# Kernel optimization log

Measured on AMD Instinct MI355X. Metric: run time of the kernel, lower is better.

Reference implementation:

```python
import jax, jax.numpy as jnp
import numpy as np
import math

NUM_BUCKETS = 32
MAX_DISTANCE = 128


def _relative_position_bucket(relative_position):
    # Unidirectional (bidirectional=False): rp = max(-relative_position, 0)
    rp = jnp.maximum(-relative_position, 0)
    max_exact = NUM_BUCKETS // 2  # 16
    is_small = rp < max_exact
    rp_f = jnp.maximum(rp, 1).astype(jnp.float32)
    large = max_exact + (
        jnp.log(rp_f / max_exact) / math.log(MAX_DISTANCE / max_exact)
        * (NUM_BUCKETS - max_exact)
    ).astype(jnp.int32)
    large = jnp.minimum(large, NUM_BUCKETS - 1)
    return jnp.where(is_small, rp, large)


def _t5_rel_bias(bias_table, T):
    # bias_table: [num_buckets, n_heads] -> [1, n_heads, T, T]
    ctx = jnp.arange(T, dtype=jnp.int32)[:, None]
    mem = jnp.arange(T, dtype=jnp.int32)[None, :]
    buckets = _relative_position_bucket(mem - ctx)  # [T, T]
    values = bias_table[buckets]  # [T, T, H]
    return jnp.transpose(values, (2, 0, 1))[None]  # [1, H, T, T]


def setup_inputs() -> dict:
    key = jax.random.key(0)
    ks = jax.random.split(key, 6)
    B, T, C, H = 2, 2048, 1024, 16
    x = jax.random.normal(ks[0], (B, T, C), dtype=jnp.float32)
    W_attn = jax.random.normal(ks[1], (C, 3 * C), dtype=jnp.float32) * 0.02
    b_attn = jnp.zeros((3 * C,), dtype=jnp.float32)
    W_proj = jax.random.normal(ks[2], (C, C), dtype=jnp.float32) * 0.02
    b_proj = jnp.zeros((C,), dtype=jnp.float32)
    bias_table = jax.random.normal(ks[3], (NUM_BUCKETS, H), dtype=jnp.float32) * 0.02
    return {"x": x, "W_attn": W_attn, "b_attn": b_attn,
            "W_proj": W_proj, "b_proj": b_proj, "bias_table": bias_table}


def reference(x, W_attn, b_attn, W_proj, b_proj, bias_table):
    B, T, C = x.shape
    H = bias_table.shape[1]
    D = C // H
    qkv = x @ W_attn + b_attn  # [B, T, 3C]
    q, k, v = jnp.split(qkv, 3, axis=-1)
    # [B, T, C] -> [B, H, T, D]
    q = q.reshape(B, T, H, D).transpose(0, 2, 1, 3)
    k = k.reshape(B, T, H, D).transpose(0, 2, 1, 3)
    v = v.reshape(B, T, H, D).transpose(0, 2, 1, 3)
    rel_bias = _t5_rel_bias(bias_table, T)  # [1, H, T, T]
    att = jnp.einsum('bhtd,bhsd->bhts', q, k) * (1.0 / math.sqrt(D))
    att = att + rel_bias
    causal = jnp.tril(jnp.ones((T, T), dtype=bool))
    att = jnp.where(causal, att, -jnp.inf)
    att = jax.nn.softmax(att, axis=-1)
    y = jnp.einsum('bhts,bhsd->bhtd', att, v)  # [B, H, T, D]
    y = y.transpose(0, 2, 1, 3).reshape(B, T, C)
    return y @ W_proj + b_proj
```

## Files before the change

kernel.cpp:

```cpp
#include <hip/hip_runtime.h>
#include <hip/hip_bf16.h>
#include <math.h>

typedef __attribute__((ext_vector_type(4))) float f32x4;
typedef __attribute__((ext_vector_type(16))) float f32x16;
typedef __attribute__((ext_vector_type(8))) __bf16 bf16x8;
typedef __attribute__((ext_vector_type(4))) __bf16 bf16x4;
typedef __attribute__((ext_vector_type(4))) unsigned int u32x4;
typedef __attribute__((ext_vector_type(2))) unsigned int u32x2;

#define DEVI __device__ __forceinline__

DEVI f32x4 mfma16(bf16x8 a, bf16x8 b, f32x4 c) {
  return __builtin_amdgcn_mfma_f32_16x16x32_bf16(a, b, c, 0, 0, 0);
}
DEVI f32x16 mfma32(bf16x8 a, bf16x8 b, f32x16 c) {
  return __builtin_amdgcn_mfma_f32_32x32x16_bf16(a, b, c, 0, 0, 0);
}

DEVI void gload16(const void* g, void* l) {
  __builtin_amdgcn_global_load_lds(
      (const __attribute__((address_space(1))) void*)g,
      (__attribute__((address_space(3))) void*)l, 16, 0, 0);
}

DEVI float exp2a(float x) {
  float r;
  asm("v_exp_f32 %0, %1" : "=v"(r) : "v"(x));
  return r;
}
DEVI unsigned cvtpk(float lo, float hi) {
  unsigned r;
  asm("v_cvt_pk_bf16_f32 %0, %1, %2" : "=v"(r) : "v"(lo), "v"(hi));
  return r;
}

#define LOG2E 1.4426950408889634f
#define QSCALE 0.18033688011110793f
#define FIXMAX 8.0f

__global__ __launch_bounds__(256) void prep_k(
    const float* __restrict__ x, const float* __restrict__ W_attn,
    const float* __restrict__ W_proj, const float* __restrict__ bt,
    __bf16* __restrict__ xb, __bf16* __restrict__ WaT,
    __bf16* __restrict__ WpT, float* __restrict__ tbl) {
  __shared__ float tile[32][33];
  int bid = blockIdx.x;
  const int t = threadIdx.x;
  if (bid < 4096) {
    int i = (bid * 256 + t) * 4;
    float4 v = *(const float4*)&x[i];
    bf16x4 o = {(__bf16)v.x, (__bf16)v.y, (__bf16)v.z, (__bf16)v.w};
    *(bf16x4*)&xb[i] = o;
    return;
  }
  bid -= 4096;
  if (bid < 4096) {
    const float* in;
    __bf16* out;
    int Cc, bx, by;
    if (bid < 3072) {
      in = W_attn; out = WaT; Cc = 3072; bx = bid % 96; by = bid / 96;
    } else {
      int b2 = bid - 3072;
      in = W_proj; out = WpT; Cc = 1024; bx = b2 % 32; by = b2 / 32;
    }
    const int R = 1024;
    int tx = t & 31, ty = t >> 5;
    int xcol = bx * 32 + tx;
    for (int r = ty; r < 32; r += 8)
      tile[r][tx] = in[(size_t)(by * 32 + r) * Cc + xcol];
    __syncthreads();
    int xo = by * 32 + tx;
    for (int r = ty; r < 32; r += 8)
      out[(size_t)(bx * 32 + r) * R + xo] = (__bf16)tile[tx][r];
    return;
  }
  bid -= 4096;
  int idx = bid * 256 + t;
  int h = idx >> 11, rp = idx & 2047;
  int bucket;
  if (rp < 16) {
    bucket = rp;
  } else {
    float v = (logf((float)rp * 0.0625f) / 2.0794415416798357f) * 16.0f;
    bucket = 16 + (int)v;
    if (bucket > 31) bucket = 31;
  }
  tbl[idx] = bt[bucket * 16 + h] * LOG2E;
}

__global__ __launch_bounds__(512, 2) void gemm_qkv(
    const __bf16* __restrict__ A, const __bf16* __restrict__ BT,
    const float* __restrict__ bias,
    __bf16* __restrict__ qb, __bf16* __restrict__ kb, __bf16* __restrict__ vtb) {
  __shared__ __align__(16) char lAm[65536];
  __shared__ __align__(16) char lBm[65536];
  const int t = threadIdx.x, w = t >> 6, lane = t & 63;
  const int wm = w >> 2, wn = w & 3;
  const int m0 = blockIdx.x * 256, n0 = blockIdx.y * 256;
  const int rA = lane & 15;
  const int aoff = rA * 128 + (((lane >> 4) * 16) ^ ((rA & 4) ? 32 : 0));
  const int bro = (wn & 1) * 8192;

  int srw[2], scl[2];
#pragma unroll
  for (int r = 0; r < 2; ++r) {
    int d = r * 8192 + w * 1024 + lane * 16;
    int lg = d ^ ((lane & 32) ? 32 : 0);
    srw[r] = lg >> 7;
    scl[r] = (lg & 127) >> 1;
  }

  f32x4 acc[8][4] = {};

  auto STG = [&](int buf, const __bf16* src, int rows0, int kk0, char* opm,
                 int half) {
#pragma unroll
    for (int r = 0; r < 2; ++r)
      gload16(src + (size_t)(rows0 + half * 128 + srw[r]) * 1024 + kk0 + scl[r],
              opm + buf * 32768 + half * 16384 + r * 8192 + w * 1024);
  };
  auto STGALL = [&](int buf, int kk0) {
    STG(buf, A, m0, kk0, lAm, 0);
    STG(buf, A, m0, kk0, lAm, 1);
    STG(buf, BT, n0, kk0, lBm, 0);
    STG(buf, BT, n0, kk0, lBm, 1);
  };

  STGALL(0, 0);
  asm volatile("s_waitcnt vmcnt(0)" ::: "memory");
  __builtin_amdgcn_s_barrier();

  for (int kt = 0; kt < 16; ++kt) {
    const int c = kt & 1;
    const char* Ah = lAm + c * 32768 + wm * 16384;
    const char* Bh = lBm + c * 32768 + (wn >> 1) * 16384 + bro;
    bf16x8 af[4][2], bfr[2][2];

#pragma unroll
    for (int i = 0; i < 4; ++i) {
      af[i][0] = *(const bf16x8*)(Ah + i * 2048 + aoff);
      af[i][1] = *(const bf16x8*)(Ah + i * 2048 + 64 + aoff);
    }
#pragma unroll
    for (int j = 0; j < 2; ++j) {
      bfr[j][0] = *(const bf16x8*)(Bh + j * 2048 + aoff);
      bfr[j][1] = *(const bf16x8*)(Bh + j * 2048 + 64 + aoff);
    }
    if (kt + 1 < 16) STGALL(c ^ 1, (kt + 1) * 64);
    __builtin_amdgcn_s_barrier();
    __builtin_amdgcn_s_setprio(1);
#pragma unroll
    for (int i = 0; i < 4; ++i)
#pragma unroll
      for (int j = 0; j < 2; ++j)
#pragma unroll
        for (int kc = 0; kc < 2; ++kc)
          acc[i][j] = mfma16(af[i][kc], bfr[j][kc], acc[i][j]);
    __builtin_amdgcn_s_setprio(0);
    __builtin_amdgcn_s_barrier();

#pragma unroll
    for (int j = 0; j < 2; ++j) {
      bfr[j][0] = *(const bf16x8*)(Bh + (2 + j) * 2048 + aoff);
      bfr[j][1] = *(const bf16x8*)(Bh + (2 + j) * 2048 + 64 + aoff);
    }
    __builtin_amdgcn_s_barrier();
    __builtin_amdgcn_s_setprio(1);
#pragma unroll
    for (int i = 0; i < 4; ++i)
#pragma unroll
      for (int j = 0; j < 2; ++j)
#pragma unroll
        for (int kc = 0; kc < 2; ++kc)
          acc[i][2 + j] = mfma16(af[i][kc], bfr[j][kc], acc[i][2 + j]);
    __builtin_amdgcn_s_setprio(0);
    __builtin_amdgcn_s_barrier();

#pragma unroll
    for (int i = 0; i < 4; ++i) {
      af[i][0] = *(const bf16x8*)(Ah + (4 + i) * 2048 + aoff);
      af[i][1] = *(const bf16x8*)(Ah + (4 + i) * 2048 + 64 + aoff);
    }
    __builtin_amdgcn_s_barrier();
    __builtin_amdgcn_s_setprio(1);
#pragma unroll
    for (int i = 0; i < 4; ++i)
#pragma unroll
      for (int j = 0; j < 2; ++j)
#pragma unroll
        for (int kc = 0; kc < 2; ++kc)
          acc[4 + i][2 + j] = mfma16(af[i][kc], bfr[j][kc], acc[4 + i][2 + j]);
    __builtin_amdgcn_s_setprio(0);
    __builtin_amdgcn_s_barrier();

#pragma unroll
    for (int j = 0; j < 2; ++j) {
      bfr[j][0] = *(const bf16x8*)(Bh + j * 2048 + aoff);
      bfr[j][1] = *(const bf16x8*)(Bh + j * 2048 + 64 + aoff);
    }
    __builtin_amdgcn_s_barrier();
    __builtin_amdgcn_s_setprio(1);
#pragma unroll
    for (int i = 0; i < 4; ++i)
#pragma unroll
      for (int j = 0; j < 2; ++j)
#pragma unroll
        for (int kc = 0; kc < 2; ++kc)
          acc[4 + i][j] = mfma16(af[i][kc], bfr[j][kc], acc[4 + i][j]);
    __builtin_amdgcn_s_setprio(0);
    if (kt + 1 < 16) asm volatile("s_waitcnt vmcnt(0)" ::: "memory");
    __builtin_amdgcn_s_barrier();
  }

#pragma unroll
  for (int j = 0; j < 4; ++j) {
    int n = n0 + wn * 64 + j * 16 + rA;
    float bv = bias[n];
    int sec = n >> 10, nn = n & 1023;
    int h = nn >> 6, d = nn & 63;
#pragma unroll
    for (int i = 0; i < 8; ++i) {
#pragma unroll
      for (int e = 0; e < 4; ++e) {
        int m = m0 + wm * 128 + i * 16 + (lane >> 4) * 4 + e;
        float v = acc[i][j][e] + bv;
        int b = m >> 11, tt = m & 2047;
        if (sec == 0)
          qb[(((size_t)(b * 16 + h)) * 2048 + tt) * 64 + d] = (__bf16)(v * QSCALE);
        else if (sec == 1)
          kb[(((size_t)(b * 16 + h)) * 2048 + tt) * 64 + d] = (__bf16)v;
        else
          vtb[(((size_t)(b * 16 + h)) * 64 + d) * 2048 + tt] = (__bf16)v;
      }
    }
  }
}

__global__ __launch_bounds__(256) void gemm_proj(
    const __bf16* __restrict__ A, const __bf16* __restrict__ BT,
    const float* __restrict__ bias, float* __restrict__ outF,
    int M, int N, int K) {
  __shared__ __align__(16) __bf16 lA[2][64 * 32];
  __shared__ __align__(16) __bf16 lB[2][128 * 32];
  const int t = threadIdx.x;
  const int w = t >> 6, lane = t & 63;
  const int m0 = blockIdx.x * 64, n0 = blockIdx.y * 128;
  const int wr = (w >> 1) * 32, wc = (w & 1) * 64;

  f32x4 acc[2][4] = {};

  const int rA = lane & 15;
  const int kk = (lane >> 4) * 8;

  auto STAGE = [&](int buf, int k0) {
    {
      int row = t >> 2, cc = t & 3;
      gload16(A + (size_t)(m0 + row) * K + k0 + cc * 8,
              &lA[buf][(w * 64) * 8]);
    }
#pragma unroll
    for (int r = 0; r < 2; ++r) {
      int c = r * 256 + t;
      int row = c >> 2, cc = c & 3;
      gload16(BT + (size_t)(n0 + row) * K + k0 + cc * 8,
              &lB[buf][(r * 256 + w * 64) * 8]);
    }
  };

  STAGE(0, 0);
  int cur = 0;
  for (int k0 = 0; k0 < K; k0 += 32, cur ^= 1) {
    __syncthreads();
    if (k0 + 32 < K) STAGE(cur ^ 1, k0 + 32);
    bf16x8 af[2], bfr[4];
#pragma unroll
    for (int i = 0; i < 2; ++i)
      af[i] = *(const bf16x8*)&lA[cur][(wr + i * 16 + rA) * 32 + kk];
#pragma unroll
    for (int j = 0; j < 4; ++j)
      bfr[j] = *(const bf16x8*)&lB[cur][(wc + j * 16 + rA) * 32 + kk];
#pragma unroll
    for (int i = 0; i < 2; ++i)
#pragma unroll
      for (int j = 0; j < 4; ++j)
        acc[i][j] = mfma16(af[i], bfr[j], acc[i][j]);
  }

  const int colb = n0 + wc + rA;
  const int rowb = m0 + wr + (lane >> 4) * 4;
#pragma unroll
  for (int j = 0; j < 4; ++j) {
    int n = colb + j * 16;
    float bv = bias[n];
#pragma unroll
    for (int i = 0; i < 2; ++i) {
#pragma unroll
      for (int e = 0; e < 4; ++e) {
        int m = rowb + i * 16 + e;
        outF[(size_t)m * N + n] = acc[i][j][e] + bv;
      }
    }
  }
}

__global__ __launch_bounds__(256) void attn_k(
    const __bf16* __restrict__ q, const __bf16* __restrict__ k,
    const __bf16* __restrict__ vt, const float* __restrict__ tbl,
    __bf16* __restrict__ y) {
  __shared__ __align__(16) char smem[2 * 8192 + 2 * 8192 + 2 * 768];
  float* lbuf = (float*)(smem + 32768);

  const int t = threadIdx.x, w = t >> 6, lane = t & 63;
  const int bh = blockIdx.x, b = bh >> 4, h = bh & 15;
  const int qt64 = 31 - blockIdx.y;
  const int qs = w >> 1, ks = w & 1;
  const int ncol = lane & 31, hi = lane >> 5;
  const int swl = ncol & 7;

  const __bf16* qp = q + (size_t)bh * 2048 * 64;
  const __bf16* kp = k + (size_t)bh * 2048 * 64;
  const __bf16* vp = vt + (size_t)bh * 64 * 2048;
  const float* tb = tbl + h * 2048;
  const float bconst = tb[2047] - FIXMAX;

  bf16x8 qf[4];
  {
    const __bf16* qr = qp + (size_t)(qt64 * 64 + qs * 32 + ncol) * 64 + hi * 8;
#pragma unroll
    for (int dc = 0; dc < 4; ++dc) qf[dc] = *(const bf16x8*)(qr + dc * 16);
  }

  f32x16 O0 = {}, O1 = {};
  float lsum = 0.f;
  const int ibase = 95 + 32 * (qs - ks) - 4 * hi + ncol;

  auto STAGE = [&](int buf, int jt) {
#pragma unroll
    for (int r = 0; r < 2; ++r) {
      int c = r * 256 + t;
      int row = c >> 3, cc = c & 7;
      int sc = cc ^ (row & 7);
      gload16(kp + (size_t)(jt * 64 + row) * 64 + sc * 8,
              smem + buf * 8192 + (r * 256 + w * 64) * 16);
      gload16(vp + (size_t)row * 2048 + jt * 64 + sc * 8,
              smem + 16384 + buf * 8192 + (r * 256 + w * 64) * 16);
    }
    int dtj = qt64 - jt;
    if (dtj < 3 && t < 192) {
      int rb = dtj * 64 - 95 + t;
      lbuf[buf * 192 + t] = tb[rb < 0 ? 0 : rb] - FIXMAX;
    }
  };

  STAGE(0, 0);
  int cur = 0;
  for (int jt = 0; jt <= qt64; ++jt, cur ^= 1) {
    const int dt = qt64 - jt;
    const int rel = 2 * dt + qs - ks;
    __syncthreads();
    if (jt < qt64) STAGE(cur ^ 1, jt + 1);
    if (rel < 0) continue;

    const char* Kc = smem + cur * 8192;
    const char* Vc = smem + 16384 + cur * 8192;
    const float* lbc = lbuf + cur * 192;

    f32x16 s;
    if (rel >= 5) {
#pragma unroll
      for (int r = 0; r < 16; ++r) s[r] = bconst;
    } else {
#pragma unroll
      for (int r = 0; r < 16; ++r) {
        int cr8 = (r & 3) + 8 * (r >> 2);
        float v = lbc[ibase - cr8];
        if (rel == 0 && ncol < cr8 + 4 * hi) v = -1e30f;
        s[r] = v;
      }
    }
    const char* Kb = Kc + (ks * 32 + ncol) * 128;
#pragma unroll
    for (int dc = 0; dc < 4; ++dc) {
      bf16x8 kf = *(const bf16x8*)(Kb + (((dc * 2 + hi) ^ swl) << 4));
      s = mfma32(kf, qf[dc], s);
    }
    float p[16];
#pragma unroll
    for (int r = 0; r < 16; ++r) {
      p[r] = exp2a(s[r]);
      lsum += p[r];
    }
#pragma unroll
    for (int s16 = 0; s16 < 2; ++s16) {
      unsigned we0 = cvtpk(p[8 * s16 + 0], p[8 * s16 + 1]);
      unsigned we1 = cvtpk(p[8 * s16 + 2], p[8 * s16 + 3]);
      unsigned wo0 = cvtpk(p[8 * s16 + 4], p[8 * s16 + 5]);
      unsigned wo1 = cvtpk(p[8 * s16 + 6], p[8 * s16 + 7]);
      u32x2 r0 = __builtin_amdgcn_permlane32_swap(we0, wo0, false, false);
      u32x2 r1 = __builtin_amdgcn_permlane32_swap(we1, wo1, false, false);
      u32x4 aw = {r0[0], r1[0], r0[1], r1[1]};
      bf16x8 af = __builtin_bit_cast(bf16x8, aw);
#pragma unroll
      for (int db = 0; db < 2; ++db) {
        const char* Vb = Vc + (db * 32 + ncol) * 128;
        bf16x8 vf = *(const bf16x8*)(Vb +
            ((((ks * 2 + s16) * 2 + hi) ^ swl) << 4));
        if (db == 0) O0 = mfma32(af, vf, O0);
        else         O1 = mfma32(af, vf, O1);
      }
    }
  }

  lsum += __shfl_xor(lsum, 32);
  __syncthreads();
  float* ls = (float*)(smem + 32768);
  if (ks) {
    char* dst = smem + qs * 8192 + lane * 128;
#pragma unroll
    for (int c = 0; c < 4; ++c) {
      f32x4 v0 = {O0[4 * c], O0[4 * c + 1], O0[4 * c + 2], O0[4 * c + 3]};
      *(f32x4*)(dst + ((c ^ swl) << 4)) = v0;
      f32x4 v1 = {O1[4 * c], O1[4 * c + 1], O1[4 * c + 2], O1[4 * c + 3]};
      *(f32x4*)(dst + (((c + 4) ^ swl) << 4)) = v1;
    }
    ls[qs * 64 + lane] = lsum;
  }
  __syncthreads();
  if (!ks) {
    lsum += ls[qs * 64 + lane];
    const char* src = smem + qs * 8192 + lane * 128;
#pragma unroll
    for (int c = 0; c < 4; ++c) {
      f32x4 v0 = *(const f32x4*)(src + ((c ^ swl) << 4));
      f32x4 v1 = *(const f32x4*)(src + (((c + 4) ^ swl) << 4));
#pragma unroll
      for (int e = 0; e < 4; ++e) {
        O0[4 * c + e] += v0[e];
        O1[4 * c + e] += v1[e];
      }
    }
    float rinv = 1.0f / lsum;
#pragma unroll
    for (int r = 0; r < 16; ++r) {
      int cr = (r & 3) + 8 * (r >> 2) + 4 * hi;
      float ri = __shfl(rinv, cr);
      int row = qt64 * 64 + qs * 32 + cr;
      size_t base = ((size_t)(b * 2048 + row)) * 1024 + h * 64 + ncol;
      y[base]      = (__bf16)(O0[r] * ri);
      y[base + 32] = (__bf16)(O1[r] * ri);
    }
  }
}


extern "C" void kernel_launch(void* const* d_in, const int* in_sizes, int n_in,
                              void* d_out, int out_size, void* d_ws, size_t ws_size,
                              hipStream_t stream) {
  const float* x = (const float*)d_in[0];
  const float* W_attn = (const float*)d_in[1];
  const float* b_attn = (const float*)d_in[2];
  const float* W_proj = (const float*)d_in[3];
  const float* b_proj = (const float*)d_in[4];
  const float* bias_table = (const float*)d_in[5];
  float* out = (float*)d_out;

  char* ws = (char*)d_ws;
  __bf16* xb   = (__bf16*)(ws + 0);
  __bf16* WaT  = (__bf16*)(ws + 8388608);
  __bf16* WpT  = (__bf16*)(ws + 14680064);
  __bf16* qb   = (__bf16*)(ws + 16777216);
  __bf16* kb   = (__bf16*)(ws + 25165824);
  __bf16* vtb  = (__bf16*)(ws + 33554432);
  __bf16* yb   = (__bf16*)(ws + 41943040);
  float*  tbl  = (float*)(ws + 50331648);

  prep_k<<<8320, 256, 0, stream>>>(x, W_attn, W_proj, bias_table,
                                   xb, WaT, WpT, tbl);
  gemm_qkv<<<dim3(16, 12), 512, 0, stream>>>(xb, WaT, b_attn, qb, kb, vtb);
  attn_k<<<dim3(32, 32), 256, 0, stream>>>(qb, kb, vtb, tbl, yb);
  gemm_proj<<<dim3(64, 8), 256, 0, stream>>>(yb, WpT, b_proj, out,
                                             4096, 1024, 1024);
}
```

Measured before the change: 133.3 us.

## Use full XOR-8 LDS swizzle and keep B fragments in registers for QKV GEMM

Changes the LDS swizzle of the QKV GEMM from a 2-way XOR to an XOR over all 8 16-byte chunks keyed by row, applied both in the global-to-LDS staging addresses and in the fragment reads, to cut LDS bank conflicts. It keeps B fragments for columns 0-1 in registers (b01) instead of reloading them, which removes one LDS reload and one barrier per k-step. The launch bound drops the 2-blocks-per-SM hint so the compiler may use more registers, at the cost of possible lower occupancy.

```diff
diff --git a/kernel.cpp b/kernel.cpp
--- a/kernel.cpp
+++ b/kernel.cpp
@@ -90,7 +90,7 @@
   tbl[idx] = bt[bucket * 16 + h] * LOG2E;
 }
 
-__global__ __launch_bounds__(512, 2) void gemm_qkv(
+__global__ __launch_bounds__(512) void gemm_qkv(
     const __bf16* __restrict__ A, const __bf16* __restrict__ BT,
     const float* __restrict__ bias,
     __bf16* __restrict__ qb, __bf16* __restrict__ kb, __bf16* __restrict__ vtb) {
@@ -100,16 +100,16 @@
   const int wm = w >> 2, wn = w & 3;
   const int m0 = blockIdx.x * 256, n0 = blockIdx.y * 256;
   const int rA = lane & 15;
-  const int aoff = rA * 128 + (((lane >> 4) * 16) ^ ((rA & 4) ? 32 : 0));
+  const int sw7 = rA & 7;
+  const int ckbase = lane >> 4;
   const int bro = (wn & 1) * 8192;
 
   int srw[2], scl[2];
 #pragma unroll
   for (int r = 0; r < 2; ++r) {
     int d = r * 8192 + w * 1024 + lane * 16;
-    int lg = d ^ ((lane & 32) ? 32 : 0);
-    srw[r] = lg >> 7;
-    scl[r] = (lg & 127) >> 1;
+    srw[r] = d >> 7;
+    scl[r] = (((d >> 4) & 7) ^ (srw[r] & 7)) * 8;
   }
 
   f32x4 acc[8][4] = {};
@@ -127,6 +127,9 @@
     STG(buf, BT, n0, kk0, lBm, 0);
     STG(buf, BT, n0, kk0, lBm, 1);
   };
+  auto FOFF = [&](int rl, int kc) {
+    return rl * 128 + (((ckbase + kc * 4) ^ sw7) << 4);
+  };
 
   STGALL(0, 0);
   asm volatile("s_waitcnt vmcnt(0)" ::: "memory");
@@ -136,18 +139,18 @@
     const int c = kt & 1;
     const char* Ah = lAm + c * 32768 + wm * 16384;
     const char* Bh = lBm + c * 32768 + (wn >> 1) * 16384 + bro;
-    bf16x8 af[4][2], bfr[2][2];
-
-#pragma unroll
-    for (int i = 0; i < 4; ++i) {
-      af[i][0] = *(const bf16x8*)(Ah + i * 2048 + aoff);
-      af[i][1] = *(const bf16x8*)(Ah + i * 2048 + 64 + aoff);
-    }
-#pragma unroll
-    for (int j = 0; j < 2; ++j) {
-      bfr[j][0] = *(const bf16x8*)(Bh + j * 2048 + aoff);
-      bfr[j][1] = *(const bf16x8*)(Bh + j * 2048 + 64 + aoff);
-    }
+    bf16x8 af[4][2], b01[2][2], b23[2][2];
+
+#pragma unroll
+    for (int i = 0; i < 4; ++i)
+#pragma unroll
+      for (int kc = 0; kc < 2; ++kc)
+        af[i][kc] = *(const bf16x8*)(Ah + FOFF(i * 16 + rA, kc));
+#pragma unroll
+    for (int j = 0; j < 2; ++j)
+#pragma unroll
+      for (int kc = 0; kc < 2; ++kc)
+        b01[j][kc] = *(const bf16x8*)(Bh + FOFF(j * 16 + rA, kc));
     if (kt + 1 < 16) STGALL(c ^ 1, (kt + 1) * 64);
     __builtin_amdgcn_s_barrier();
     __builtin_amdgcn_s_setprio(1);
@@ -157,15 +160,15 @@
       for (int j = 0; j < 2; ++j)
 #pragma unroll
         for (int kc = 0; kc < 2; ++kc)
-          acc[i][j] = mfma16(af[i][kc], bfr[j][kc], acc[i][j]);
+          acc[i][j] = mfma16(af[i][kc], b01[j][kc], acc[i][j]);
     __builtin_amdgcn_s_setprio(0);
     __builtin_amdgcn_s_barrier();
 
 #pragma unroll
-    for (int j = 0; j < 2; ++j) {
-      bfr[j][0] = *(const bf16x8*)(Bh + (2 + j) * 2048 + aoff);
-      bfr[j][1] = *(const bf16x8*)(Bh + (2 + j) * 2048 + 64 + aoff);
-    }
+    for (int j = 0; j < 2; ++j)
+#pragma unroll
+      for (int kc = 0; kc < 2; ++kc)
+        b23[j][kc] = *(const bf16x8*)(Bh + FOFF((2 + j) * 16 + rA, kc));
     __builtin_amdgcn_s_barrier();
     __builtin_amdgcn_s_setprio(1);
 #pragma unroll
@@ -174,15 +177,15 @@
       for (int j = 0; j < 2; ++j)
 #pragma unroll
         for (int kc = 0; kc < 2; ++kc)
-          acc[i][2 + j] = mfma16(af[i][kc], bfr[j][kc], acc[i][2 + j]);
+          acc[i][2 + j] = mfma16(af[i][kc], b23[j][kc], acc[i][2 + j]);
     __builtin_amdgcn_s_setprio(0);
     __builtin_amdgcn_s_barrier();
 
 #pragma unroll
-    for (int i = 0; i < 4; ++i) {
-      af[i][0] = *(const bf16x8*)(Ah + (4 + i) * 2048 + aoff);
-      af[i][1] = *(const bf16x8*)(Ah + (4 + i) * 2048 + 64 + aoff);
-    }
+    for (int i = 0; i < 4; ++i)
+#pragma unroll
+      for (int kc = 0; kc < 2; ++kc)
+        af[i][kc] = *(const bf16x8*)(Ah + FOFF((4 + i) * 16 + rA, kc));
     __builtin_amdgcn_s_barrier();
     __builtin_amdgcn_s_setprio(1);
 #pragma unroll
@@ -191,16 +194,10 @@
       for (int j = 0; j < 2; ++j)
 #pragma unroll
         for (int kc = 0; kc < 2; ++kc)
-          acc[4 + i][2 + j] = mfma16(af[i][kc], bfr[j][kc], acc[4 + i][2 + j]);
+          acc[4 + i][2 + j] = mfma16(af[i][kc], b23[j][kc], acc[4 + i][2 + j]);
     __builtin_amdgcn_s_setprio(0);
     __builtin_amdgcn_s_barrier();
 
-#pragma unroll
-    for (int j = 0; j < 2; ++j) {
-      bfr[j][0] = *(const bf16x8*)(Bh + j * 2048 + aoff);
-      bfr[j][1] = *(const bf16x8*)(Bh + j * 2048 + 64 + aoff);
-    }
-    __builtin_amdgcn_s_barrier();
     __builtin_amdgcn_s_setprio(1);
 #pragma unroll
     for (int i = 0; i < 4; ++i)
@@ -208,7 +205,7 @@
       for (int j = 0; j < 2; ++j)
 #pragma unroll
         for (int kc = 0; kc < 2; ++kc)
-          acc[4 + i][j] = mfma16(af[i][kc], bfr[j][kc], acc[4 + i][j]);
+          acc[4 + i][j] = mfma16(af[i][kc], b01[j][kc], acc[4 + i][j]);
     __builtin_amdgcn_s_setprio(0);
     if (kt + 1 < 16) asm volatile("s_waitcnt vmcnt(0)" ::: "memory");
     __builtin_amdgcn_s_barrier();
```

Measured after the change: 131.0 us. About the same (-1.8%).
